# Performance work log

Measured on AMD Instinct MI355X. Metric: run time of the kernel, lower is better.

Reference implementation:

```python
import jax, jax.numpy as jnp
import numpy as np
from math import sqrt

B, S, D = 4, 2048, 1024


def setup_inputs() -> dict:
    key = jax.random.key(0)
    k1, k2, k3, k4 = jax.random.split(key, 4)
    scale = 1.0 / sqrt(D)  # roughly nn.Linear init magnitude
    x = jax.random.normal(k1, (B, S, D), dtype=jnp.float32)
    Wq = jax.random.normal(k2, (D, D), dtype=jnp.float32) * scale
    Wk = jax.random.normal(k3, (D, D), dtype=jnp.float32) * scale
    Wv = jax.random.normal(k4, (D, D), dtype=jnp.float32) * scale
    attn_mask = jnp.ones((B, S), dtype=jnp.int32)  # 1 = attend, 0 = pad
    return {"x": x, "attn_mask": attn_mask, "Wq": Wq, "Wk": Wk, "Wv": Wv}


def reference(x, attn_mask, Wq, Wk, Wv):
    # torch nn.Linear: y = x @ W.T (no bias)
    q = jnp.einsum("bsd,ed->bse", x, Wq)
    k = jnp.einsum("bsd,ed->bse", x, Wk)
    v = jnp.einsum("bsd,ed->bse", x, Wv)

    scores = jnp.einsum("bqd,bkd->bqk", q, k)  # [B, S, S]

    # causal mask (upper triangle above diagonal masked out)
    causal_mask = jnp.triu(jnp.ones((S, S), dtype=bool), k=1)  # [S, S]
    scores = jnp.where(causal_mask[None, :, :], -jnp.inf, scores)

    # padding mask: attn_mask [B, S] broadcast over query dim
    pad = (attn_mask == 0)[:, None, :]  # [B, 1, S]
    scores = jnp.where(pad, -jnp.inf, scores)

    attn_weights = jax.nn.softmax(scores / sqrt(D), axis=-1)
    return jnp.einsum("bqk,bkd->bqd", attn_weights, v)
```

## Files before the change

kernel.cpp:

```cpp
#include <hip/hip_runtime.h>
#include <stdint.h>
#include <math.h>

#define BK 64
#define LSTR 64
#define ETS 132

typedef __attribute__((ext_vector_type(8))) short short8;
typedef __attribute__((ext_vector_type(16))) float floatx16;

typedef __attribute__((address_space(3))) unsigned int lds_u32;
typedef const __attribute__((address_space(1))) unsigned int glb_u32;

__device__ __forceinline__ unsigned short f2bf(float f) {
    union { float f; unsigned u; } x; x.f = f;
    unsigned r = x.u + 0x7fffu + ((x.u >> 16) & 1u);
    return (unsigned short)(r >> 16);
}

__global__ void cvt_kernel(const float* __restrict__ x,
                           const float* __restrict__ wq,
                           const float* __restrict__ wk,
                           const float* __restrict__ wv,
                           unsigned short* __restrict__ xb,
                           unsigned short* __restrict__ wb,
                           float* __restrict__ lsum) {
    int i4 = (blockIdx.x * 256 + threadIdx.x) * 4;
    if (blockIdx.x < 8) {
        float4 z = (float4){0.f, 0.f, 0.f, 0.f};
        *(float4*)(lsum + i4) = z;
    }
    const float* src; unsigned short* dst; int off;
    if (i4 < 8388608)       { src = x;  dst = xb;            off = i4; }
    else if (i4 < 9437184)  { src = wq; dst = wb;            off = i4 - 8388608; }
    else if (i4 < 10485760) { src = wk; dst = wb + 1048576;  off = i4 - 9437184; }
    else                    { src = wv; dst = wb + 2097152;  off = i4 - 10485760; }
    float4 v = *(const float4*)(src + off);
    ushort4 o;
    o.x = f2bf(v.x); o.y = f2bf(v.y); o.z = f2bf(v.z); o.w = f2bf(v.w);
    *(ushort4*)(dst + off) = o;
}

__device__ __forceinline__ void stage_async(unsigned short* sh, const unsigned short* g,
                                            int ld, int tid) {
#pragma unroll
    for (int it = 0; it < 4; ++it) {
        int c = it * 256 + tid;
        int row = c >> 3, cc = c & 7;
        int gcc = cc ^ (row & 7);
        __builtin_amdgcn_global_load_lds(
            (glb_u32*)(g + (size_t)row * ld + gcc * 8),
            (lds_u32*)(sh + c * 8), 16, 0, 0);
    }
}

__device__ __forceinline__ void mfma_step(const unsigned short* Ash, const unsigned short* Bsh,
                                          int lane, int wr, int wc, floatx16 acc[2][2]) {
    int lm = lane & 31, lg = lane >> 5;
#pragma unroll
    for (int h = 0; h < 4; ++h) {
        short8 af[2], bf[2];
#pragma unroll
        for (int i = 0; i < 2; ++i) {
            int ar = wr * 64 + i * 32 + lm;
            int br = wc * 64 + i * 32 + lm;
            af[i] = *(const short8*)(Ash + ar * LSTR + (((h << 1) | lg) ^ (ar & 7)) * 8);
            bf[i] = *(const short8*)(Bsh + br * LSTR + (((h << 1) | lg) ^ (br & 7)) * 8);
        }
#pragma unroll
        for (int i = 0; i < 2; ++i)
#pragma unroll
            for (int j = 0; j < 2; ++j)
                acc[i][j] = __builtin_amdgcn_mfma_f32_32x32x16_bf16(af[i], bf[j], acc[i][j], 0, 0, 0);
    }
}

#define ACC_ZERO {0.f,0.f,0.f,0.f,0.f,0.f,0.f,0.f,0.f,0.f,0.f,0.f,0.f,0.f,0.f,0.f}


__global__ __launch_bounds__(256) void qkv_gemm(const unsigned short* __restrict__ Xb,
                                                const unsigned short* __restrict__ Wb,
                                                unsigned short* __restrict__ Qb,
                                                unsigned short* __restrict__ Kb,
                                                unsigned short* __restrict__ Vt) {
    __shared__ unsigned short shbuf[128 * ETS];
    unsigned short* Ash = shbuf;
    unsigned short* Bsh = shbuf + 128 * LSTR;
    int tid = threadIdx.x;
    int bm = blockIdx.x, bn = blockIdx.y;
    int lane = tid & 63, w = tid >> 6, wr = w >> 1, wc = w & 1;
    floatx16 acc[2][2] = {{ACC_ZERO, ACC_ZERO}, {ACC_ZERO, ACC_ZERO}};

    const unsigned short* Ag = Xb + (size_t)bm * 128 * 1024;
    const unsigned short* Bg = Wb + (size_t)bn * 128 * 1024;
    for (int k0 = 0; k0 < 1024; k0 += BK) {
        __syncthreads();
        stage_async(Ash, Ag + k0, 1024, tid);
        stage_async(Bsh, Bg + k0, 1024, tid);
        __syncthreads();
        mfma_step(Ash, Bsh, lane, wr, wc, acc);
    }

    int which = bn >> 3;
    int nnb = (bn & 7) * 128;
    int lm = lane & 31, lg = lane >> 5;
    __syncthreads();
    if (which < 2) {
#pragma unroll
        for (int i = 0; i < 2; ++i)
#pragma unroll
            for (int j = 0; j < 2; ++j)
#pragma unroll
                for (int p = 0; p < 16; ++p) {
                    int row = wr * 64 + i * 32 + (p & 3) + 8 * (p >> 2) + 4 * lg;
                    shbuf[row * ETS + wc * 64 + j * 32 + lm] = f2bf(acc[i][j][p]);
                }
    } else {
#pragma unroll
        for (int i = 0; i < 2; ++i)
#pragma unroll
            for (int j = 0; j < 2; ++j)
#pragma unroll
                for (int g = 0; g < 4; ++g) {
                    int mb = wr * 64 + i * 32 + 8 * g + 4 * lg;
                    ushort4 o;
                    o.x = f2bf(acc[i][j][4 * g + 0]); o.y = f2bf(acc[i][j][4 * g + 1]);
                    o.z = f2bf(acc[i][j][4 * g + 2]); o.w = f2bf(acc[i][j][4 * g + 3]);
                    *(ushort4*)(shbuf + (wc * 64 + j * 32 + lm) * ETS + mb) = o;
                }
    }
    __syncthreads();

    unsigned short* gbase; size_t gld;
    if (which == 0)      { gbase = Qb + (size_t)(bm * 128) * 1024 + nnb; gld = 1024; }
    else if (which == 1) { gbase = Kb + (size_t)(bm * 128) * 1024 + nnb; gld = 1024; }
    else { gbase = Vt + ((size_t)(bm >> 4) * 1024 + nnb) * 2048 + (bm & 15) * 128; gld = 2048; }
#pragma unroll
    for (int it = 0; it < 4; ++it) {
        int row = it * 32 + (tid >> 3), cc = tid & 7;
        uint4 v0 = *(const uint4*)(shbuf + row * ETS + cc * 8);
        uint4 v1 = *(const uint4*)(shbuf + row * ETS + 64 + cc * 8);
        *(uint4*)(gbase + (size_t)row * gld + cc * 8) = v0;
        *(uint4*)(gbase + (size_t)row * gld + 64 + cc * 8) = v1;
    }
}

__global__ __launch_bounds__(256) void scores_gemm(const unsigned short* __restrict__ Qb,
                                                   const unsigned short* __restrict__ Kb,
                                                   const int* __restrict__ mask,
                                                   unsigned short* __restrict__ Pb,
                                                   float* __restrict__ lsum) {
    int u = blockIdx.x, b = blockIdx.y;
    int ti = (int)((sqrtf(8.0f * (float)u + 1.0f) - 1.0f) * 0.5f);
    while ((ti + 1) * (ti + 2) / 2 <= u) ti++;
    while (ti * (ti + 1) / 2 > u) ti--;
    int tj = u - ti * (ti + 1) / 2;

    __shared__ unsigned short shbuf[128 * ETS];
    unsigned short* Ash = shbuf;
    unsigned short* Bsh = shbuf + 128 * LSTR;
    int tid = threadIdx.x;
    int lane = tid & 63, w = tid >> 6, wr = w >> 1, wc = w & 1;
    floatx16 acc[2][2] = {{ACC_ZERO, ACC_ZERO}, {ACC_ZERO, ACC_ZERO}};

    const unsigned short* Ag = Qb + ((size_t)b * 2048 + ti * 128) * 1024;
    const unsigned short* Bg = Kb + ((size_t)b * 2048 + tj * 128) * 1024;
    for (int k0 = 0; k0 < 1024; k0 += BK) {
        __syncthreads();
        stage_async(Ash, Ag + k0, 1024, tid);
        stage_async(Bsh, Bg + k0, 1024, tid);
        __syncthreads();
        mfma_step(Ash, Bsh, lane, wr, wc, acc);
    }

    int lm = lane & 31, lg = lane >> 5;
    int mk[2];
#pragma unroll
    for (int j = 0; j < 2; ++j)
        mk[j] = mask[b * 2048 + tj * 128 + wc * 64 + j * 32 + lm];

    __syncthreads();
    float* lrow_sum = lsum + b * 2048;
#pragma unroll
    for (int i = 0; i < 2; ++i) {
#pragma unroll
        for (int p = 0; p < 16; ++p) {
            int rloc = wr * 64 + i * 32 + (p & 3) + 8 * (p >> 2) + 4 * lg;
            int q = ti * 128 + rloc;
            float rs = 0.f;
#pragma unroll
            for (int j = 0; j < 2; ++j) {
                int n = tj * 128 + wc * 64 + j * 32 + lm;
                float pv = 0.f;
                if (n <= q && mk[j] != 0) pv = __expf(acc[i][j][p] * 0.03125f);
                rs += pv;
                shbuf[rloc * ETS + wc * 64 + j * 32 + lm] = f2bf(pv);
            }
#pragma unroll
            for (int o = 1; o <= 16; o <<= 1) rs += __shfl_xor(rs, o);
            if (lm == 0) atomicAdd(&lrow_sum[q], rs);
        }
    }
    __syncthreads();

    unsigned short* gbase = Pb + ((size_t)b * 2048 + ti * 128) * 2048 + tj * 128;
#pragma unroll
    for (int it = 0; it < 4; ++it) {
        int row = it * 32 + (tid >> 3), cc = tid & 7;
        uint4 v0 = *(const uint4*)(shbuf + row * ETS + cc * 8);
        uint4 v1 = *(const uint4*)(shbuf + row * ETS + 64 + cc * 8);
        *(uint4*)(gbase + (size_t)row * 2048 + cc * 8) = v0;
        *(uint4*)(gbase + (size_t)row * 2048 + 64 + cc * 8) = v1;
    }
}

__global__ __launch_bounds__(256) void pv_gemm(const unsigned short* __restrict__ Pb,
                                               const unsigned short* __restrict__ Vt,
                                               const float* __restrict__ lsum,
                                               float* __restrict__ out) {
    int bid = blockIdx.x;
    int half = bid >> 8, rr = bid & 255;
    int tig = rr >> 5;
    int ti = half ? tig : 15 - tig;
    int dj = (rr >> 2) & 7;
    int b  = rr & 3;
    __shared__ unsigned short shbuf[2 * 128 * LSTR];
    unsigned short* Ash = shbuf;
    unsigned short* Bsh = shbuf + 128 * LSTR;
    int tid = threadIdx.x;
    int lane = tid & 63, w = tid >> 6, wr = w >> 1, wc = w & 1;
    floatx16 acc[2][2] = {{ACC_ZERO, ACC_ZERO}, {ACC_ZERO, ACC_ZERO}};

    const unsigned short* Ag = Pb + ((size_t)b * 2048 + ti * 128) * 2048;
    const unsigned short* Bg = Vt + ((size_t)b * 1024 + dj * 128) * 2048;
    int kend = (ti + 1) * 128;
    for (int k0 = 0; k0 < kend; k0 += BK) {
        __syncthreads();
        stage_async(Ash, Ag + k0, 2048, tid);
        stage_async(Bsh, Bg + k0, 2048, tid);
        __syncthreads();
        mfma_step(Ash, Bsh, lane, wr, wc, acc);
    }

    int lm = lane & 31, lg = lane >> 5;
#pragma unroll
    for (int i = 0; i < 2; ++i) {
#pragma unroll
        for (int g = 0; g < 4; ++g) {
            int qb = ti * 128 + wr * 64 + i * 32 + 8 * g + 4 * lg;
#pragma unroll
            for (int r = 0; r < 4; ++r) {
                float invl = 1.f / lsum[b * 2048 + qb + r];
#pragma unroll
                for (int j = 0; j < 2; ++j) {
                    int d = dj * 128 + wc * 64 + j * 32 + lm;
                    out[((size_t)b * 2048 + qb + r) * 1024 + d] = acc[i][j][4 * g + r] * invl;
                }
            }
        }
    }
}

extern "C" void kernel_launch(void* const* d_in, const int* in_sizes, int n_in,
                              void* d_out, int out_size, void* d_ws, size_t ws_size,
                              hipStream_t stream) {
    const float* x    = (const float*)d_in[0];
    const int*   mask = (const int*)d_in[1];
    const float* wq   = (const float*)d_in[2];
    const float* wk   = (const float*)d_in[3];
    const float* wv   = (const float*)d_in[4];
    float* out = (float*)d_out;
    char* ws = (char*)d_ws;

    unsigned short* Xb = (unsigned short*)(ws + 0);
    unsigned short* Wb = (unsigned short*)(ws + 16777216);
    unsigned short* Qb = (unsigned short*)(ws + 23068672);
    unsigned short* Kb = (unsigned short*)(ws + 39845888);
    unsigned short* Vt = (unsigned short*)(ws + 56623104);
    unsigned short* Pb = (unsigned short*)(ws + 73400320);
    float*        lsum = (float*)(ws + 106954752);
    (void)ws_size; (void)in_sizes; (void)n_in; (void)out_size;

    cvt_kernel<<<11264, 256, 0, stream>>>(x, wq, wk, wv, Xb, Wb, lsum);
    qkv_gemm<<<dim3(64, 24), 256, 0, stream>>>(Xb, Wb, Qb, Kb, Vt);
    scores_gemm<<<dim3(136, 4), 256, 0, stream>>>(Qb, Kb, mask, Pb, lsum);
    pv_gemm<<<512, 256, 0, stream>>>(Pb, Vt, lsum, out);
}
```

Measured before the change: 235.4 us.

## Rewrite QKV projection GEMM with 256x256 tiles and double-buffered LDS pipeline

The QKV projection GEMM moves from 128x128 tiles with 256 threads to 256x256 tiles with 512 threads (8 waves, each computing 128x64). Global-to-LDS async loads are double-buffered, so the next K-slice is prefetched while MFMAs run on the current one, and setprio raises priority around the MFMA bursts. The goal is more operand reuse per loaded byte and hiding load latency behind compute. In exchange the kernel uses a larger LDS footprint (128KB) and more accumulator registers, and launches only 384 blocks, which may not fill the CUs evenly. The epilogue is split into two halves to reuse LDS.

```diff
diff --git a/kernel.cpp b/kernel.cpp
--- a/kernel.cpp
+++ b/kernel.cpp
@@ -5,6 +5,7 @@
 #define BK 64
 #define LSTR 64
 #define ETS 132
+#define QTILE 16384
 
 typedef __attribute__((ext_vector_type(8))) short short8;
 typedef __attribute__((ext_vector_type(16))) float floatx16;
@@ -78,70 +79,146 @@
 #define ACC_ZERO {0.f,0.f,0.f,0.f,0.f,0.f,0.f,0.f,0.f,0.f,0.f,0.f,0.f,0.f,0.f,0.f}
 
 
-__global__ __launch_bounds__(256) void qkv_gemm(const unsigned short* __restrict__ Xb,
-                                                const unsigned short* __restrict__ Wb,
-                                                unsigned short* __restrict__ Qb,
-                                                unsigned short* __restrict__ Kb,
-                                                unsigned short* __restrict__ Vt) {
-    __shared__ unsigned short shbuf[128 * ETS];
-    unsigned short* Ash = shbuf;
-    unsigned short* Bsh = shbuf + 128 * LSTR;
+__device__ __forceinline__ void stage256(unsigned short* sh, const unsigned short* g, int tid) {
+#pragma unroll
+    for (int it = 0; it < 4; ++it) {
+        int c = it * 512 + tid;
+        int row = c >> 3, cc = c & 7;
+        int gcc = cc ^ (row & 7);
+        __builtin_amdgcn_global_load_lds(
+            (glb_u32*)(g + (size_t)row * 1024 + gcc * 8),
+            (lds_u32*)(sh + c * 8), 16, 0, 0);
+    }
+}
+
+__global__ __launch_bounds__(512, 2) void qkv_gemm(const unsigned short* __restrict__ Xb,
+                                                   const unsigned short* __restrict__ Wb,
+                                                   unsigned short* __restrict__ Qb,
+                                                   unsigned short* __restrict__ Kb,
+                                                   unsigned short* __restrict__ Vt) {
+    __shared__ unsigned short lds[4 * QTILE];
     int tid = threadIdx.x;
     int bm = blockIdx.x, bn = blockIdx.y;
-    int lane = tid & 63, w = tid >> 6, wr = w >> 1, wc = w & 1;
-    floatx16 acc[2][2] = {{ACC_ZERO, ACC_ZERO}, {ACC_ZERO, ACC_ZERO}};
-
-    const unsigned short* Ag = Xb + (size_t)bm * 128 * 1024;
-    const unsigned short* Bg = Wb + (size_t)bn * 128 * 1024;
-    for (int k0 = 0; k0 < 1024; k0 += BK) {
-        __syncthreads();
-        stage_async(Ash, Ag + k0, 1024, tid);
-        stage_async(Bsh, Bg + k0, 1024, tid);
-        __syncthreads();
-        mfma_step(Ash, Bsh, lane, wr, wc, acc);
-    }
-
-    int which = bn >> 3;
-    int nnb = (bn & 7) * 128;
+    int lane = tid & 63, w = tid >> 6;
+    int wm = w >> 2, wn = w & 3;
     int lm = lane & 31, lg = lane >> 5;
-    __syncthreads();
+    int xr = lm & 7;
+
+    floatx16 acc[4][2];
+#pragma unroll
+    for (int mi = 0; mi < 4; ++mi)
+#pragma unroll
+        for (int nj = 0; nj < 2; ++nj)
+            acc[mi][nj] = (floatx16)0.f;
+
+    int aoff[4], boff[2];
+#pragma unroll
+    for (int mi = 0; mi < 4; ++mi) aoff[mi] = (wm * 128 + mi * 32 + lm) * LSTR;
+#pragma unroll
+    for (int nj = 0; nj < 2; ++nj) boff[nj] = (wn * 64 + nj * 32 + lm) * LSTR;
+
+    const unsigned short* Ag = Xb + (size_t)bm * 256 * 1024;
+    const unsigned short* Bg = Wb + (size_t)bn * 256 * 1024;
+
+    stage256(lds, Ag, tid);
+    stage256(lds + 2 * QTILE, Bg, tid);
+    asm volatile("s_waitcnt vmcnt(0)" ::: "memory");
+    __builtin_amdgcn_s_barrier();
+    __builtin_amdgcn_sched_barrier(0);
+
+    int cur = 0;
+#pragma unroll 2
+    for (int t = 0; t < 16; ++t) {
+        const unsigned short* Ash = lds + cur * QTILE;
+        const unsigned short* Bsh = lds + 2 * QTILE + cur * QTILE;
+        if (t < 15) {
+            stage256(lds + (cur ^ 1) * QTILE, Ag + (t + 1) * BK, tid);
+            stage256(lds + 2 * QTILE + (cur ^ 1) * QTILE, Bg + (t + 1) * BK, tid);
+        }
+#pragma unroll
+        for (int h = 0; h < 4; ++h) {
+            int co = ((((h << 1) | lg) ^ xr)) << 3;
+            short8 af[4], bf[2];
+#pragma unroll
+            for (int mi = 0; mi < 4; ++mi)
+                af[mi] = *(const short8*)(Ash + aoff[mi] + co);
+#pragma unroll
+            for (int nj = 0; nj < 2; ++nj)
+                bf[nj] = *(const short8*)(Bsh + boff[nj] + co);
+            __builtin_amdgcn_s_barrier();
+            __builtin_amdgcn_s_setprio(1);
+#pragma unroll
+            for (int mi = 0; mi < 4; ++mi)
+#pragma unroll
+                for (int nj = 0; nj < 2; ++nj)
+                    acc[mi][nj] = __builtin_amdgcn_mfma_f32_32x32x16_bf16(af[mi], bf[nj], acc[mi][nj], 0, 0, 0);
+            __builtin_amdgcn_s_setprio(0);
+            if (h < 3) __builtin_amdgcn_s_barrier();
+        }
+        if (t < 15) { asm volatile("s_waitcnt vmcnt(0)" ::: "memory"); }
+        __builtin_amdgcn_s_barrier();
+        __builtin_amdgcn_sched_barrier(0);
+        cur ^= 1;
+    }
+
+    int which = bn >> 2;
+    int nnb = (bn & 3) << 8;
+    unsigned short* ep = lds;
+    const int EPS = 136;
     if (which < 2) {
-#pragma unroll
-        for (int i = 0; i < 2; ++i)
-#pragma unroll
-            for (int j = 0; j < 2; ++j)
-#pragma unroll
-                for (int p = 0; p < 16; ++p) {
-                    int row = wr * 64 + i * 32 + (p & 3) + 8 * (p >> 2) + 4 * lg;
-                    shbuf[row * ETS + wc * 64 + j * 32 + lm] = f2bf(acc[i][j][p]);
-                }
+        unsigned short* gq = (which == 0 ? Qb : Kb) + (size_t)bm * 256 * 1024 + nnb;
+#pragma unroll
+        for (int c = 0; c < 2; ++c) {
+            __syncthreads();
+            if ((wn >> 1) == c) {
+                int colb = (wn & 1) * 64;
+#pragma unroll
+                for (int mi = 0; mi < 4; ++mi)
+#pragma unroll
+                    for (int nj = 0; nj < 2; ++nj)
+#pragma unroll
+                        for (int p = 0; p < 16; ++p) {
+                            int m = wm * 128 + mi * 32 + (p & 3) + 8 * (p >> 2) + 4 * lg;
+                            ep[m * EPS + colb + nj * 32 + lm] = f2bf(acc[mi][nj][p]);
+                        }
+            }
+            __syncthreads();
+#pragma unroll
+            for (int it = 0; it < 8; ++it) {
+                int m = it * 32 + (tid >> 4), cg = tid & 15;
+                *(uint4*)(gq + (size_t)m * 1024 + c * 128 + cg * 8) =
+                    *(const uint4*)(ep + m * EPS + cg * 8);
+            }
+        }
     } else {
-#pragma unroll
-        for (int i = 0; i < 2; ++i)
-#pragma unroll
-            for (int j = 0; j < 2; ++j)
-#pragma unroll
-                for (int g = 0; g < 4; ++g) {
-                    int mb = wr * 64 + i * 32 + 8 * g + 4 * lg;
-                    ushort4 o;
-                    o.x = f2bf(acc[i][j][4 * g + 0]); o.y = f2bf(acc[i][j][4 * g + 1]);
-                    o.z = f2bf(acc[i][j][4 * g + 2]); o.w = f2bf(acc[i][j][4 * g + 3]);
-                    *(ushort4*)(shbuf + (wc * 64 + j * 32 + lm) * ETS + mb) = o;
-                }
-    }
-    __syncthreads();
-
-    unsigned short* gbase; size_t gld;
-    if (which == 0)      { gbase = Qb + (size_t)(bm * 128) * 1024 + nnb; gld = 1024; }
-    else if (which == 1) { gbase = Kb + (size_t)(bm * 128) * 1024 + nnb; gld = 1024; }
-    else { gbase = Vt + ((size_t)(bm >> 4) * 1024 + nnb) * 2048 + (bm & 15) * 128; gld = 2048; }
-#pragma unroll
-    for (int it = 0; it < 4; ++it) {
-        int row = it * 32 + (tid >> 3), cc = tid & 7;
-        uint4 v0 = *(const uint4*)(shbuf + row * ETS + cc * 8);
-        uint4 v1 = *(const uint4*)(shbuf + row * ETS + 64 + cc * 8);
-        *(uint4*)(gbase + (size_t)row * gld + cc * 8) = v0;
-        *(uint4*)(gbase + (size_t)row * gld + 64 + cc * 8) = v1;
+        unsigned short* gv = Vt + ((size_t)(bm >> 3) * 1024 + nnb) * 2048 + (bm & 7) * 256;
+#pragma unroll
+        for (int c = 0; c < 2; ++c) {
+            __syncthreads();
+            if (wm == c) {
+#pragma unroll
+                for (int mi = 0; mi < 4; ++mi)
+#pragma unroll
+                    for (int nj = 0; nj < 2; ++nj) {
+                        int n = wn * 64 + nj * 32 + lm;
+#pragma unroll
+                        for (int g = 0; g < 4; ++g) {
+                            int mloc = mi * 32 + 8 * g + 4 * lg;
+                            ushort4 o;
+                            o.x = f2bf(acc[mi][nj][4 * g + 0]); o.y = f2bf(acc[mi][nj][4 * g + 1]);
+                            o.z = f2bf(acc[mi][nj][4 * g + 2]); o.w = f2bf(acc[mi][nj][4 * g + 3]);
+                            *(ushort4*)(ep + n * EPS + mloc) = o;
+                        }
+                    }
+            }
+            __syncthreads();
+#pragma unroll
+            for (int it = 0; it < 8; ++it) {
+                int n = it * 32 + (tid >> 4), mg = tid & 15;
+                *(uint4*)(gv + (size_t)n * 2048 + c * 128 + mg * 8) =
+                    *(const uint4*)(ep + n * EPS + mg * 8);
+            }
+        }
     }
 }
 
@@ -282,7 +359,7 @@
     (void)ws_size; (void)in_sizes; (void)n_in; (void)out_size;
 
     cvt_kernel<<<11264, 256, 0, stream>>>(x, wq, wk, wv, Xb, Wb, lsum);
-    qkv_gemm<<<dim3(64, 24), 256, 0, stream>>>(Xb, Wb, Qb, Kb, Vt);
+    qkv_gemm<<<dim3(32, 12), 512, 0, stream>>>(Xb, Wb, Qb, Kb, Vt);
     scores_gemm<<<dim3(136, 4), 256, 0, stream>>>(Qb, Kb, mask, Pb, lsum);
     pv_gemm<<<512, 256, 0, stream>>>(Pb, Vt, lsum, out);
 }
```

After: 246.1 us. 4.5% more time.

## Double-buffer LDS tiles with async prefetch in all three GEMM kernels

Applied to the files above, without the earlier changes.

Converts the QKV, scores and PV GEMM main loops from single-buffered staging into double-buffered LDS. The next K-tile is issued asynchronously into the alternate buffer while MFMAs run on the current one, with one barrier per iteration instead of two. The goal is to hide global-to-LDS latency behind compute. In exchange, LDS per block grows to 64 KB, which may lower occupancy. Correctness also depends on the async loads having completed by the time the barrier is reached.

```diff
diff --git a/kernel.cpp b/kernel.cpp
--- a/kernel.cpp
+++ b/kernel.cpp
@@ -5,6 +5,7 @@
 #define BK 64
 #define LSTR 64
 #define ETS 132
+#define TSH 8192
 
 typedef __attribute__((ext_vector_type(8))) short short8;
 typedef __attribute__((ext_vector_type(16))) float floatx16;
@@ -83,9 +84,7 @@
                                                 unsigned short* __restrict__ Qb,
                                                 unsigned short* __restrict__ Kb,
                                                 unsigned short* __restrict__ Vt) {
-    __shared__ unsigned short shbuf[128 * ETS];
-    unsigned short* Ash = shbuf;
-    unsigned short* Bsh = shbuf + 128 * LSTR;
+    __shared__ unsigned short shbuf[4 * TSH];
     int tid = threadIdx.x;
     int bm = blockIdx.x, bn = blockIdx.y;
     int lane = tid & 63, w = tid >> 6, wr = w >> 1, wc = w & 1;
@@ -93,18 +92,25 @@
 
     const unsigned short* Ag = Xb + (size_t)bm * 128 * 1024;
     const unsigned short* Bg = Wb + (size_t)bn * 128 * 1024;
-    for (int k0 = 0; k0 < 1024; k0 += BK) {
+    stage_async(shbuf, Ag, 1024, tid);
+    stage_async(shbuf + 2 * TSH, Bg, 1024, tid);
+    __syncthreads();
+#pragma unroll 2
+    for (int t = 0; t < 16; ++t) {
+        int cur = t & 1;
+        unsigned short* Ash = shbuf + cur * TSH;
+        unsigned short* Bsh = shbuf + (2 + cur) * TSH;
+        if (t < 15) {
+            stage_async(shbuf + (cur ^ 1) * TSH, Ag + (t + 1) * BK, 1024, tid);
+            stage_async(shbuf + (2 + (cur ^ 1)) * TSH, Bg + (t + 1) * BK, 1024, tid);
+        }
+        mfma_step(Ash, Bsh, lane, wr, wc, acc);
         __syncthreads();
-        stage_async(Ash, Ag + k0, 1024, tid);
-        stage_async(Bsh, Bg + k0, 1024, tid);
-        __syncthreads();
-        mfma_step(Ash, Bsh, lane, wr, wc, acc);
     }
 
     int which = bn >> 3;
     int nnb = (bn & 7) * 128;
     int lm = lane & 31, lg = lane >> 5;
-    __syncthreads();
     if (which < 2) {
 #pragma unroll
         for (int i = 0; i < 2; ++i)
@@ -156,21 +162,27 @@
     while (ti * (ti + 1) / 2 > u) ti--;
     int tj = u - ti * (ti + 1) / 2;
 
-    __shared__ unsigned short shbuf[128 * ETS];
-    unsigned short* Ash = shbuf;
-    unsigned short* Bsh = shbuf + 128 * LSTR;
+    __shared__ unsigned short shbuf[4 * TSH];
     int tid = threadIdx.x;
     int lane = tid & 63, w = tid >> 6, wr = w >> 1, wc = w & 1;
     floatx16 acc[2][2] = {{ACC_ZERO, ACC_ZERO}, {ACC_ZERO, ACC_ZERO}};
 
     const unsigned short* Ag = Qb + ((size_t)b * 2048 + ti * 128) * 1024;
     const unsigned short* Bg = Kb + ((size_t)b * 2048 + tj * 128) * 1024;
-    for (int k0 = 0; k0 < 1024; k0 += BK) {
+    stage_async(shbuf, Ag, 1024, tid);
+    stage_async(shbuf + 2 * TSH, Bg, 1024, tid);
+    __syncthreads();
+#pragma unroll 2
+    for (int t = 0; t < 16; ++t) {
+        int cur = t & 1;
+        unsigned short* Ash = shbuf + cur * TSH;
+        unsigned short* Bsh = shbuf + (2 + cur) * TSH;
+        if (t < 15) {
+            stage_async(shbuf + (cur ^ 1) * TSH, Ag + (t + 1) * BK, 1024, tid);
+            stage_async(shbuf + (2 + (cur ^ 1)) * TSH, Bg + (t + 1) * BK, 1024, tid);
+        }
+        mfma_step(Ash, Bsh, lane, wr, wc, acc);
         __syncthreads();
-        stage_async(Ash, Ag + k0, 1024, tid);
-        stage_async(Bsh, Bg + k0, 1024, tid);
-        __syncthreads();
-        mfma_step(Ash, Bsh, lane, wr, wc, acc);
     }
 
     int lm = lane & 31, lg = lane >> 5;
@@ -179,7 +191,6 @@
     for (int j = 0; j < 2; ++j)
         mk[j] = mask[b * 2048 + tj * 128 + wc * 64 + j * 32 + lm];
 
-    __syncthreads();
     float* lrow_sum = lsum + b * 2048;
 #pragma unroll
     for (int i = 0; i < 2; ++i) {
@@ -224,22 +235,27 @@
     int ti = half ? tig : 15 - tig;
     int dj = (rr >> 2) & 7;
     int b  = rr & 3;
-    __shared__ unsigned short shbuf[2 * 128 * LSTR];
-    unsigned short* Ash = shbuf;
-    unsigned short* Bsh = shbuf + 128 * LSTR;
+    __shared__ unsigned short shbuf[4 * TSH];
     int tid = threadIdx.x;
     int lane = tid & 63, w = tid >> 6, wr = w >> 1, wc = w & 1;
     floatx16 acc[2][2] = {{ACC_ZERO, ACC_ZERO}, {ACC_ZERO, ACC_ZERO}};
 
     const unsigned short* Ag = Pb + ((size_t)b * 2048 + ti * 128) * 2048;
     const unsigned short* Bg = Vt + ((size_t)b * 1024 + dj * 128) * 2048;
-    int kend = (ti + 1) * 128;
-    for (int k0 = 0; k0 < kend; k0 += BK) {
+    int nt = (ti + 1) * 2;
+    stage_async(shbuf, Ag, 2048, tid);
+    stage_async(shbuf + 2 * TSH, Bg, 2048, tid);
+    __syncthreads();
+    for (int t = 0; t < nt; ++t) {
+        int cur = t & 1;
+        unsigned short* Ash = shbuf + cur * TSH;
+        unsigned short* Bsh = shbuf + (2 + cur) * TSH;
+        if (t + 1 < nt) {
+            stage_async(shbuf + (cur ^ 1) * TSH, Ag + (t + 1) * BK, 2048, tid);
+            stage_async(shbuf + (2 + (cur ^ 1)) * TSH, Bg + (t + 1) * BK, 2048, tid);
+        }
+        mfma_step(Ash, Bsh, lane, wr, wc, acc);
         __syncthreads();
-        stage_async(Ash, Ag + k0, 2048, tid);
-        stage_async(Bsh, Bg + k0, 2048, tid);
-        __syncthreads();
-        mfma_step(Ash, Bsh, lane, wr, wc, acc);
     }
 
     int lm = lane & 31, lg = lane >> 5;
```

Measured after the change: 229.1 us. 2.7% less time.
